# Performance work log

Measured on AMD Instinct MI355X. Metric: run time of the kernel, lower is better.

The kernel has to match this reference:

```python
import jax, jax.numpy as jnp
import numpy as np


def setup_inputs() -> dict:
    key = jax.random.key(0)
    ks = jax.random.split(key, 8)
    B, C, H, W = 4, 512, 64, 64
    M = C // 8
    sq = 1.0 / np.sqrt(C)
    return {
        "x": jax.random.normal(ks[0], (B, C, H, W), jnp.float32),
        "Wq": jax.random.normal(ks[1], (M, C), jnp.float32) * sq,
        "bq": jnp.zeros((M,), jnp.float32),
        "Wk": jax.random.normal(ks[2], (M, C), jnp.float32) * sq,
        "bk": jnp.zeros((M,), jnp.float32),
        "Wv": jax.random.normal(ks[3], (C, C), jnp.float32) * sq,
        "bv": jnp.zeros((C,), jnp.float32),
        "gamma": jax.random.uniform(ks[4], (1,), jnp.float32),
    }


def reference(x, Wq, bq, Wk, bk, Wv, bv, gamma):
    B, C, H, W = x.shape
    N = H * W
    xf = x.reshape(B, C, N)  # flatten spatial -> [B, C, N]
    # 1x1 convs are channel-mixing matmuls
    q = jnp.einsum('mc,bcn->bmn', Wq, xf) + bq[None, :, None]  # [B, M, N]
    k = jnp.einsum('mc,bcn->bmn', Wk, xf) + bk[None, :, None]  # [B, M, N]
    v = jnp.einsum('dc,bcn->bdn', Wv, xf) + bv[None, :, None]  # [B, C, N]
    # sim[b,i,j] = <q[:, i], k[:, j]>, softmax over j
    sim = jnp.einsum('bmi,bmj->bij', q, k)  # [B, N, N]
    attn = jax.nn.softmax(sim, axis=-1)
    # feat[b,c,i] = sum_j v[b,c,j] * attn[b,i,j]
    feat = jnp.einsum('bcj,bij->bci', v, attn)  # [B, C, N]
    out = gamma[0] * feat.reshape(B, C, H, W) + x
    return out
```

## Files before the change

### kernel.cpp

```cpp
#include <hip/hip_runtime.h>

typedef _Float16 f16;
typedef _Float16 f16x8 __attribute__((ext_vector_type(8)));
typedef float    f32x4 __attribute__((ext_vector_type(4)));
typedef unsigned int u32x2 __attribute__((ext_vector_type(2)));

#define B_ 4
#define C_ 512
#define N_ 4096
#define M_ 64

__device__ __forceinline__ unsigned pk2(float a, float b) {
    union { f16 h[2]; unsigned u; } t;
    t.h[0] = (f16)a; t.h[1] = (f16)b;
    return t.u;
}

__global__ __launch_bounds__(256) void wcvt(
    const float* __restrict__ Wq, const float* __restrict__ Wk,
    const float* __restrict__ Wv, f16* __restrict__ Wf)
{
    const int e = (blockIdx.x * 256 + threadIdx.x) * 8;
    const float* src;
    int off;
    if (e < 32768)      { src = Wq; off = e; }
    else if (e < 65536) { src = Wk; off = e - 32768; }
    else                { src = Wv; off = e - 65536; }
    float4 a = *(const float4*)(src + off);
    float4 b = *(const float4*)(src + off + 4);
    f16x8 o;
    o[0]=(f16)a.x; o[1]=(f16)a.y; o[2]=(f16)a.z; o[3]=(f16)a.w;
    o[4]=(f16)b.x; o[5]=(f16)b.y; o[6]=(f16)b.z; o[7]=(f16)b.w;
    *(f16x8*)(Wf + e) = o;
}

__global__ __launch_bounds__(512) void qkv2(
    const f16* __restrict__ Wf, const float* __restrict__ x,
    const float* __restrict__ bq, const float* __restrict__ bk,
    const float* __restrict__ bv,
    f16* __restrict__ qt, f16* __restrict__ ktf, f16* __restrict__ vf)
{
    __shared__ float sX[2][64][65];
    __shared__ float sBias[640];

    const int tid  = threadIdx.x;
    const int w    = tid >> 6;
    const int lane = tid & 63;
    const int l15  = lane & 15;
    const int quad = lane >> 4;
    const int n0   = blockIdx.x * 64;
    const int b    = blockIdx.y;
    const int row0 = w * 80;

    for (int e = tid; e < 640; e += 512)
        sBias[e] = (e < 64) ? bq[e] : (e < 128) ? bk[e - 64] : bv[e - 128];

    {
        float4 g[2];
        #pragma unroll
        for (int i = 0; i < 2; ++i) {
            int e = i * 512 + tid, c = e >> 4, n4 = (e & 15) * 4;
            g[i] = *(const float4*)(x + ((size_t)(b * C_ + c)) * N_ + n0 + n4);
        }
        #pragma unroll
        for (int i = 0; i < 2; ++i) {
            int e = i * 512 + tid, c = e >> 4, n4 = (e & 15) * 4;
            sX[0][c][n4 + 0] = g[i].x; sX[0][c][n4 + 1] = g[i].y;
            sX[0][c][n4 + 2] = g[i].z; sX[0][c][n4 + 3] = g[i].w;
        }
    }

    f32x4 acc[5][4] = {};

    for (int t = 0; t < 8; ++t) {
        const int cur = t & 1, nxt = cur ^ 1;

        float4 gn[2];
        if (t < 7) {
            #pragma unroll
            for (int i = 0; i < 2; ++i) {
                int e = i * 512 + tid, c = e >> 4, n4 = (e & 15) * 4;
                gn[i] = *(const float4*)(x + ((size_t)(b * C_ + (t + 1) * 64 + c)) * N_ + n0 + n4);
            }
        }

        __syncthreads();

        f16x8 af[5][2];
        #pragma unroll
        for (int ot = 0; ot < 5; ++ot)
            #pragma unroll
            for (int kh = 0; kh < 2; ++kh)
                af[ot][kh] = *(const f16x8*)(Wf + (size_t)(row0 + ot * 16 + l15) * 512
                                             + t * 64 + kh * 32 + quad * 8);

        f16x8 bf[4][2];
        #pragma unroll
        for (int nt = 0; nt < 4; ++nt)
            #pragma unroll
            for (int kh = 0; kh < 2; ++kh) {
                f16x8 o;
                #pragma unroll
                for (int jj = 0; jj < 8; ++jj)
                    o[jj] = (f16)sX[cur][kh * 32 + quad * 8 + jj][nt * 16 + l15];
                bf[nt][kh] = o;
            }

        #pragma unroll
        for (int ot = 0; ot < 5; ++ot)
            #pragma unroll
            for (int kh = 0; kh < 2; ++kh)
                #pragma unroll
                for (int nt = 0; nt < 4; ++nt)
                    acc[ot][nt] = __builtin_amdgcn_mfma_f32_16x16x32_f16(
                        af[ot][kh], bf[nt][kh], acc[ot][nt], 0, 0, 0);

        if (t < 7) {
            #pragma unroll
            for (int i = 0; i < 2; ++i) {
                int e = i * 512 + tid, c = e >> 4, n4 = (e & 15) * 4;
                sX[nxt][c][n4 + 0] = gn[i].x; sX[nxt][c][n4 + 1] = gn[i].y;
                sX[nxt][c][n4 + 2] = gn[i].z; sX[nxt][c][n4 + 3] = gn[i].w;
            }
        }
    }

    #pragma unroll
    for (int ot = 0; ot < 5; ++ot) {
        const int rowBase = row0 + ot * 16;
        const int rq = rowBase + quad * 4;
        #pragma unroll
        for (int nt = 0; nt < 4; ++nt) {
            const int n = n0 + nt * 16 + l15;
            union { f16 h[4]; unsigned long long u; } pkv;
            #pragma unroll
            for (int r = 0; r < 4; ++r)
                pkv.h[r] = (f16)(acc[ot][nt][r] + sBias[rq + r]);
            if (rowBase < 64) {
                *(unsigned long long*)(qt + ((size_t)(b * N_ + n)) * M_ + rq) = pkv.u;
            } else if (rowBase < 128) {
                const int ol = rq - 64;
                size_t idx = (((size_t)b * 256 + (n >> 4)) * 2 + (ol >> 5)) * 512
                           + (size_t)((((ol >> 3) & 3) * 16 + (n & 15)) * 8) + (ol & 7);
                *(unsigned long long*)(ktf + idx) = pkv.u;
            } else {
                const int c = rq - 128;
                #pragma unroll
                for (int r = 0; r < 4; ++r) {
                    size_t idx = ((size_t)b * (C_ * N_)) + (size_t)((c + r) >> 4) * 65536
                               + (size_t)(n >> 6) * 1024 + (size_t)((n >> 5) & 1) * 512
                               + (size_t)((((n >> 3) & 3) * 16 + ((c + r) & 15)) * 8) + (n & 7);
                    vf[idx] = pkv.h[r];
                }
            }
        }
    }
}

__global__ __launch_bounds__(512, 2) void attn(
    const f16* __restrict__ qt, const f16* __restrict__ ktf,
    const f16* __restrict__ vf, const float* __restrict__ x,
    const float* __restrict__ gamma, float* __restrict__ out)
{
    __shared__ __align__(16) char Pb[2][8192];
    __shared__ float mxs[8][4][16];
    __shared__ float lss[8][4][16];

    const int tid  = threadIdx.x;
    const int w    = tid >> 6;
    const int lane = tid & 63;
    const int l15  = lane & 15;
    const int quad = lane >> 4;
    const int jt   = w & 3;
    const int ish  = w >> 2;
    const int is0  = ish * 2, is1 = is0 + 1;

    const int lin  = blockIdx.x;
    const int b    = (lin & 7) >> 1;
    const int iblk = ((lin >> 3) << 1) | (lin & 1);
    const int i0   = iblk * 64;

    const f16* kln = ktf + (size_t)b * (N_ * M_) + lane * 8;
    const f16* vln = vf  + (size_t)b * (C_ * N_) + lane * 8;

    f16x8 bqf[4][2];
    #pragma unroll
    for (int is = 0; is < 4; ++is)
        #pragma unroll
        for (int kh = 0; kh < 2; ++kh)
            bqf[is][kh] = *(const f16x8*)(qt + ((size_t)(b * N_ + i0 + is * 16 + l15)) * M_
                                          + kh * 32 + quad * 8);

    float mx[4];
    #pragma unroll
    for (int is = 0; is < 4; ++is) mx[is] = -3.0e38f;
    {
        const f16* kw = kln + (size_t)(w * 512) * 64;
        f16x8 akc[4][2];
        #pragma unroll
        for (int t = 0; t < 4; ++t)
            #pragma unroll
            for (int kh = 0; kh < 2; ++kh)
                akc[t][kh] = *(const f16x8*)(kw + t * 1024 + kh * 512);

        #pragma unroll 2
        for (int jj = 0; jj < 512; jj += 64) {
            f16x8 akn[4][2];
            if (jj + 64 < 512) {
                const f16* kn = kw + (size_t)(jj + 64) * 64;
                #pragma unroll
                for (int t = 0; t < 4; ++t)
                    #pragma unroll
                    for (int kh = 0; kh < 2; ++kh)
                        akn[t][kh] = *(const f16x8*)(kn + t * 1024 + kh * 512);
            }
            #pragma unroll
            for (int t = 0; t < 4; ++t) {
                #pragma unroll
                for (int is = 0; is < 4; ++is) {
                    f32x4 s = {};
                    s = __builtin_amdgcn_mfma_f32_16x16x32_f16(akc[t][0], bqf[is][0], s, 0, 0, 0);
                    s = __builtin_amdgcn_mfma_f32_16x16x32_f16(akc[t][1], bqf[is][1], s, 0, 0, 0);
                    mx[is] = fmaxf(mx[is], fmaxf(fmaxf(s[0], s[1]), fmaxf(s[2], s[3])));
                }
            }
            #pragma unroll
            for (int t = 0; t < 4; ++t)
                #pragma unroll
                for (int kh = 0; kh < 2; ++kh)
                    akc[t][kh] = akn[t][kh];
        }
    }
    #pragma unroll
    for (int is = 0; is < 4; ++is) {
        mx[is] = fmaxf(mx[is], __shfl_xor(mx[is], 16, 64));
        mx[is] = fmaxf(mx[is], __shfl_xor(mx[is], 32, 64));
    }
    if (lane < 16) {
        #pragma unroll
        for (int is = 0; is < 4; ++is) mxs[w][is][lane] = mx[is];
    }
    __syncthreads();
    float m0 = -3.0e38f, m1 = -3.0e38f;
    #pragma unroll
    for (int w2 = 0; w2 < 8; ++w2) {
        m0 = fmaxf(m0, mxs[w2][is0][l15]);
        m1 = fmaxf(m1, mxs[w2][is1][l15]);
    }

    f32x4 acc[4][4] = {};
    float lp0 = 0.f, lp1 = 0.f;

    char* pbB = (char*)&Pb[0][0];
    const int swz = (l15 & 7) << 4;
    const int wb0 = ((is0 * 16 + l15) * 128 + (jt * 16 + quad * 4) * 2) ^ swz;
    const int wb1 = wb0 + 2048;
    int rb[4][2];
    #pragma unroll
    for (int is = 0; is < 4; ++is)
        #pragma unroll
        for (int kh = 0; kh < 2; ++kh)
            rb[is][kh] = ((is * 16 + l15) * 128 + kh * 64 + quad * 16) ^ swz;

    const f16* kp = kln + (size_t)(jt * 16) * 64;
    const int cw = w * 4;

    f16x8 ak0 = *(const f16x8*)(kp);
    f16x8 ak1 = *(const f16x8*)(kp + 512);
    {
        f32x4 s0 = {}, s1 = {};
        s0 = __builtin_amdgcn_mfma_f32_16x16x32_f16(ak0, bqf[is0][0], s0, 0, 0, 0);
        s0 = __builtin_amdgcn_mfma_f32_16x16x32_f16(ak1, bqf[is0][1], s0, 0, 0, 0);
        s1 = __builtin_amdgcn_mfma_f32_16x16x32_f16(ak0, bqf[is1][0], s1, 0, 0, 0);
        s1 = __builtin_amdgcn_mfma_f32_16x16x32_f16(ak1, bqf[is1][1], s1, 0, 0, 0);
        float p0 = __expf(s0[0] - m0), p1 = __expf(s0[1] - m0);
        float p2 = __expf(s0[2] - m0), p3 = __expf(s0[3] - m0);
        lp0 += (p0 + p1) + (p2 + p3);
        u32x2 pw0 = { pk2(p0, p1), pk2(p2, p3) };
        *(u32x2*)(pbB + wb0) = pw0;
        float q0 = __expf(s1[0] - m1), q1 = __expf(s1[1] - m1);
        float q2 = __expf(s1[2] - m1), q3 = __expf(s1[3] - m1);
        lp1 += (q0 + q1) + (q2 + q3);
        u32x2 pw1 = { pk2(q0, q1), pk2(q2, q3) };
        *(u32x2*)(pbB + wb1) = pw1;
    }
    ak0 = *(const f16x8*)(kp + 4096);
    ak1 = *(const f16x8*)(kp + 4096 + 512);
    f16x8 vc0[4], vc1[4];
    #pragma unroll
    for (int ct = 0; ct < 4; ++ct) {
        vc0[ct] = *(const f16x8*)(vln + (size_t)(cw + ct) * 65536);
        vc1[ct] = *(const f16x8*)(vln + (size_t)(cw + ct) * 65536 + 512);
    }
    __syncthreads();

    #pragma unroll 2
    for (int t = 0; t < 63; ++t) {
        const int cb = (t & 1) * 8192;
        const int nb = ((t + 1) & 1) * 8192;

        f16x8 pbf[4][2];
        #pragma unroll
        for (int is = 0; is < 4; ++is)
            #pragma unroll
            for (int kh = 0; kh < 2; ++kh)
                pbf[is][kh] = *(const f16x8*)(pbB + cb + rb[is][kh]);

        f32x4 s0 = {}, s1 = {};
        s0 = __builtin_amdgcn_mfma_f32_16x16x32_f16(ak0, bqf[is0][0], s0, 0, 0, 0);
        s0 = __builtin_amdgcn_mfma_f32_16x16x32_f16(ak1, bqf[is0][1], s0, 0, 0, 0);
        s1 = __builtin_amdgcn_mfma_f32_16x16x32_f16(ak0, bqf[is1][0], s1, 0, 0, 0);
        s1 = __builtin_amdgcn_mfma_f32_16x16x32_f16(ak1, bqf[is1][1], s1, 0, 0, 0);

        if (t + 2 < 64) {
            ak0 = *(const f16x8*)(kp + (size_t)(t + 2) * 4096);
            ak1 = *(const f16x8*)(kp + (size_t)(t + 2) * 4096 + 512);
        }
        const f16* vt = vln + (size_t)(t + 1) * 1024;
        f16x8 vn0[4], vn1[4];
        #pragma unroll
        for (int ct = 0; ct < 4; ++ct) {
            vn0[ct] = *(const f16x8*)(vt + (size_t)(cw + ct) * 65536);
            vn1[ct] = *(const f16x8*)(vt + (size_t)(cw + ct) * 65536 + 512);
        }

        {
            float p0 = __expf(s0[0] - m0), p1 = __expf(s0[1] - m0);
            float p2 = __expf(s0[2] - m0), p3 = __expf(s0[3] - m0);
            lp0 += (p0 + p1) + (p2 + p3);
            u32x2 pw = { pk2(p0, p1), pk2(p2, p3) };
            *(u32x2*)(pbB + nb + wb0) = pw;
        }
        {
            float q0 = __expf(s1[0] - m1), q1 = __expf(s1[1] - m1);
            float q2 = __expf(s1[2] - m1), q3 = __expf(s1[3] - m1);
            lp1 += (q0 + q1) + (q2 + q3);
            u32x2 pw = { pk2(q0, q1), pk2(q2, q3) };
            *(u32x2*)(pbB + nb + wb1) = pw;
        }

        __builtin_amdgcn_s_setprio(1);
        #pragma unroll
        for (int ct = 0; ct < 4; ++ct)
            #pragma unroll
            for (int is = 0; is < 4; ++is)
                acc[ct][is] = __builtin_amdgcn_mfma_f32_16x16x32_f16(vc0[ct], pbf[is][0], acc[ct][is], 0, 0, 0);
        #pragma unroll
        for (int ct = 0; ct < 4; ++ct)
            #pragma unroll
            for (int is = 0; is < 4; ++is)
                acc[ct][is] = __builtin_amdgcn_mfma_f32_16x16x32_f16(vc1[ct], pbf[is][1], acc[ct][is], 0, 0, 0);
        __builtin_amdgcn_s_setprio(0);

        __syncthreads();

        #pragma unroll
        for (int ct = 0; ct < 4; ++ct) { vc0[ct] = vn0[ct]; vc1[ct] = vn1[ct]; }
    }

    {
        const int cb = (63 & 1) * 8192;
        f16x8 pbf[4][2];
        #pragma unroll
        for (int is = 0; is < 4; ++is)
            #pragma unroll
            for (int kh = 0; kh < 2; ++kh)
                pbf[is][kh] = *(const f16x8*)(pbB + cb + rb[is][kh]);
        #pragma unroll
        for (int ct = 0; ct < 4; ++ct)
            #pragma unroll
            for (int is = 0; is < 4; ++is)
                acc[ct][is] = __builtin_amdgcn_mfma_f32_16x16x32_f16(vc0[ct], pbf[is][0], acc[ct][is], 0, 0, 0);
        #pragma unroll
        for (int ct = 0; ct < 4; ++ct)
            #pragma unroll
            for (int is = 0; is < 4; ++is)
                acc[ct][is] = __builtin_amdgcn_mfma_f32_16x16x32_f16(vc1[ct], pbf[is][1], acc[ct][is], 0, 0, 0);
    }

    lp0 += __shfl_xor(lp0, 16, 64);
    lp0 += __shfl_xor(lp0, 32, 64);
    lp1 += __shfl_xor(lp1, 16, 64);
    lp1 += __shfl_xor(lp1, 32, 64);
    if (lane < 16) { lss[w][is0][lane] = lp0; lss[w][is1][lane] = lp1; }
    __syncthreads();

    float linv[4];
    #pragma unroll
    for (int is = 0; is < 4; ++is) {
        const int wb = (is >> 1) * 4;
        float l = (lss[wb + 0][is][l15] + lss[wb + 1][is][l15])
                + (lss[wb + 2][is][l15] + lss[wb + 3][is][l15]);
        linv[is] = 1.0f / l;
    }

    const float g = gamma[0];
    #pragma unroll
    for (int is = 0; is < 4; ++is) {
        const int i = i0 + is * 16 + l15;
        #pragma unroll
        for (int ct = 0; ct < 4; ++ct) {
            #pragma unroll
            for (int r = 0; r < 4; ++r) {
                const int c = w * 64 + ct * 16 + quad * 4 + r;
                const size_t idx = ((size_t)(b * C_ + c)) * N_ + i;
                out[idx] = g * (acc[ct][is][r] * linv[is]) + x[idx];
            }
        }
    }
}

extern "C" void kernel_launch(void* const* d_in, const int* in_sizes, int n_in,
                              void* d_out, int out_size, void* d_ws, size_t ws_size,
                              hipStream_t stream)
{
    const float* x     = (const float*)d_in[0];
    const float* Wq    = (const float*)d_in[1];
    const float* bq    = (const float*)d_in[2];
    const float* Wk    = (const float*)d_in[3];
    const float* bk    = (const float*)d_in[4];
    const float* Wv    = (const float*)d_in[5];
    const float* bv    = (const float*)d_in[6];
    const float* gamma = (const float*)d_in[7];
    float* out = (float*)d_out;

    char* ws = (char*)d_ws;
    f16* qt  = (f16*)ws;
    f16* ktf = qt + (size_t)B_ * N_ * M_;
    f16* vf  = ktf + (size_t)B_ * N_ * M_;
    f16* Wf  = vf + (size_t)B_ * C_ * N_;

    wcvt<<<dim3(160), 256, 0, stream>>>(Wq, Wk, Wv, Wf);
    qkv2<<<dim3(N_ / 64, B_), 512, 0, stream>>>(Wf, x, bq, bk, bv, qt, ktf, vf);
    attn<<<dim3(256), 512, 0, stream>>>(qt, ktf, vf, x, gamma, out);
}
```

Measured before the change: 224.2 us.

## Store x tile as swizzled fp16 in LDS and prefetch weight fragments

The qkv projection kernel now converts x to fp16 before staging it in shared memory. Each thread loads 8 channels for one spatial column, which it writes as a single 16-byte vector into an XOR-swizzled layout, so B fragments come back as one vector LDS read instead of eight scalar float reads with conversions. Weight A fragments for the next k-step are also prefetched into registers and double-buffered alongside the x tile. This adds register pressure, and the global loads of x become scalar per-lane reads instead of float4.

```diff
diff --git a/kernel.cpp b/kernel.cpp
--- a/kernel.cpp
+++ b/kernel.cpp
@@ -40,7 +40,7 @@
     const float* __restrict__ bv,
     f16* __restrict__ qt, f16* __restrict__ ktf, f16* __restrict__ vf)
 {
-    __shared__ float sX[2][64][65];
+    __shared__ __align__(16) char sH[2][8192];
     __shared__ float sBias[640];
 
     const int tid  = threadIdx.x;
@@ -55,56 +55,64 @@
     for (int e = tid; e < 640; e += 512)
         sBias[e] = (e < 64) ? bq[e] : (e < 128) ? bk[e - 64] : bv[e - 128];
 
+    const int wbyte = (lane * 128 + w * 16) ^ ((lane & 7) << 4);
+    int rbyte[4][2];
+    #pragma unroll
+    for (int nt = 0; nt < 4; ++nt) {
+        const int n = nt * 16 + l15;
+        #pragma unroll
+        for (int kh = 0; kh < 2; ++kh)
+            rbyte[nt][kh] = (n * 128 + kh * 64 + quad * 16) ^ ((n & 7) << 4);
+    }
+
+    const float* xg = x + (size_t)b * (C_ * N_) + n0 + lane;
+    const f16*   wp = Wf + (size_t)row0 * 512 + quad * 8;
+
     {
-        float4 g[2];
-        #pragma unroll
-        for (int i = 0; i < 2; ++i) {
-            int e = i * 512 + tid, c = e >> 4, n4 = (e & 15) * 4;
-            g[i] = *(const float4*)(x + ((size_t)(b * C_ + c)) * N_ + n0 + n4);
-        }
-        #pragma unroll
-        for (int i = 0; i < 2; ++i) {
-            int e = i * 512 + tid, c = e >> 4, n4 = (e & 15) * 4;
-            sX[0][c][n4 + 0] = g[i].x; sX[0][c][n4 + 1] = g[i].y;
-            sX[0][c][n4 + 2] = g[i].z; sX[0][c][n4 + 3] = g[i].w;
-        }
-    }
+        float g[8];
+        #pragma unroll
+        for (int u = 0; u < 8; ++u)
+            g[u] = xg[(size_t)(w * 8 + u) * N_];
+        f16x8 h;
+        #pragma unroll
+        for (int u = 0; u < 8; ++u) h[u] = (f16)g[u];
+        *(f16x8*)(&sH[0][0] + wbyte) = h;
+    }
+    f16x8 afc[5][2];
+    #pragma unroll
+    for (int ot = 0; ot < 5; ++ot)
+        #pragma unroll
+        for (int kh = 0; kh < 2; ++kh)
+            afc[ot][kh] = *(const f16x8*)(wp + (size_t)(ot * 16 + l15) * 512 + kh * 32);
 
     f32x4 acc[5][4] = {};
 
     for (int t = 0; t < 8; ++t) {
-        const int cur = t & 1, nxt = cur ^ 1;
-
-        float4 gn[2];
+        char* sc = &sH[t & 1][0];
+        char* sn = &sH[(t & 1) ^ 1][0];
+
+        float gn[8];
+        f16x8 afn[5][2];
         if (t < 7) {
             #pragma unroll
-            for (int i = 0; i < 2; ++i) {
-                int e = i * 512 + tid, c = e >> 4, n4 = (e & 15) * 4;
-                gn[i] = *(const float4*)(x + ((size_t)(b * C_ + (t + 1) * 64 + c)) * N_ + n0 + n4);
-            }
+            for (int u = 0; u < 8; ++u)
+                gn[u] = xg[(size_t)((t + 1) * 64 + w * 8 + u) * N_];
+            #pragma unroll
+            for (int ot = 0; ot < 5; ++ot)
+                #pragma unroll
+                for (int kh = 0; kh < 2; ++kh)
+                    afn[ot][kh] = *(const f16x8*)(wp + (size_t)(ot * 16 + l15) * 512
+                                                  + (t + 1) * 64 + kh * 32);
         }
 
         __syncthreads();
 
-        f16x8 af[5][2];
-        #pragma unroll
-        for (int ot = 0; ot < 5; ++ot)
+        f16x8 bf[4][2];
+        #pragma unroll
+        for (int nt = 0; nt < 4; ++nt)
             #pragma unroll
             for (int kh = 0; kh < 2; ++kh)
-                af[ot][kh] = *(const f16x8*)(Wf + (size_t)(row0 + ot * 16 + l15) * 512
-                                             + t * 64 + kh * 32 + quad * 8);
-
-        f16x8 bf[4][2];
-        #pragma unroll
-        for (int nt = 0; nt < 4; ++nt)
-            #pragma unroll
-            for (int kh = 0; kh < 2; ++kh) {
-                f16x8 o;
-                #pragma unroll
-                for (int jj = 0; jj < 8; ++jj)
-                    o[jj] = (f16)sX[cur][kh * 32 + quad * 8 + jj][nt * 16 + l15];
-                bf[nt][kh] = o;
-            }
+                bf[nt][kh] = *(const f16x8*)(sc + rbyte[nt][kh]);
 
         #pragma unroll
         for (int ot = 0; ot < 5; ++ot)
@@ -113,15 +121,18 @@
                 #pragma unroll
                 for (int nt = 0; nt < 4; ++nt)
                     acc[ot][nt] = __builtin_amdgcn_mfma_f32_16x16x32_f16(
-                        af[ot][kh], bf[nt][kh], acc[ot][nt], 0, 0, 0);
+                        afc[ot][kh], bf[nt][kh], acc[ot][nt], 0, 0, 0);
 
         if (t < 7) {
-            #pragma unroll
-            for (int i = 0; i < 2; ++i) {
-                int e = i * 512 + tid, c = e >> 4, n4 = (e & 15) * 4;
-                sX[nxt][c][n4 + 0] = gn[i].x; sX[nxt][c][n4 + 1] = gn[i].y;
-                sX[nxt][c][n4 + 2] = gn[i].z; sX[nxt][c][n4 + 3] = gn[i].w;
-            }
+            f16x8 h;
+            #pragma unroll
+            for (int u = 0; u < 8; ++u) h[u] = (f16)gn[u];
+            *(f16x8*)(sn + wbyte) = h;
+            #pragma unroll
+            for (int ot = 0; ot < 5; ++ot)
+                #pragma unroll
+                for (int kh = 0; kh < 2; ++kh)
+                    afc[ot][kh] = afn[ot][kh];
         }
     }
 
```

After: 215.2 us. -4.0%, faster.

## Halve QKV projection tile and stage x as swizzled fp16 in shared memory

Applied to the files above, without the earlier changes.

The QKV projection kernel now processes 32 spatial positions per block instead of 64, which doubles the grid to 512 blocks and raises occupancy via launch bounds. The x tile is converted to fp16 once when stored and kept in an XOR-swizzled byte layout, so B fragments become single vector LDS reads instead of eight scalar float reads plus conversions. Weight fragments are loaded per output tile inside the loop to cut register pressure. In exchange, every weight fragment is reloaded twice as often across blocks, and global x loads become scalar strided reads.

```diff
diff --git a/kernel.cpp b/kernel.cpp
--- a/kernel.cpp
+++ b/kernel.cpp
@@ -1,6 +1,7 @@
 #include <hip/hip_runtime.h>
 
 typedef _Float16 f16;
+typedef _Float16 f16x4 __attribute__((ext_vector_type(4)));
 typedef _Float16 f16x8 __attribute__((ext_vector_type(8)));
 typedef float    f32x4 __attribute__((ext_vector_type(4)));
 typedef unsigned int u32x2 __attribute__((ext_vector_type(2)));
@@ -34,13 +35,13 @@
     *(f16x8*)(Wf + e) = o;
 }
 
-__global__ __launch_bounds__(512) void qkv2(
+__global__ __launch_bounds__(512, 4) void qkv3(
     const f16* __restrict__ Wf, const float* __restrict__ x,
     const float* __restrict__ bq, const float* __restrict__ bk,
     const float* __restrict__ bv,
     f16* __restrict__ qt, f16* __restrict__ ktf, f16* __restrict__ vf)
 {
-    __shared__ float sX[2][64][65];
+    __shared__ __align__(16) char sH[2][4096];
     __shared__ float sBias[640];
 
     const int tid  = threadIdx.x;
@@ -48,80 +49,78 @@
     const int lane = tid & 63;
     const int l15  = lane & 15;
     const int quad = lane >> 4;
-    const int n0   = blockIdx.x * 64;
+    const int n0   = blockIdx.x * 32;
     const int b    = blockIdx.y;
     const int row0 = w * 80;
 
     for (int e = tid; e < 640; e += 512)
         sBias[e] = (e < 64) ? bq[e] : (e < 128) ? bk[e - 64] : bv[e - 128];
 
+    const int sn  = tid & 31;
+    const int scg = tid >> 5;
+    const int wbyte = (sn * 128 + scg * 8) ^ ((sn & 7) << 4);
+    int rbyte[2][2];
+    #pragma unroll
+    for (int nt = 0; nt < 2; ++nt)
+        #pragma unroll
+        for (int kh = 0; kh < 2; ++kh)
+            rbyte[nt][kh] = ((nt * 16 + l15) * 128 + kh * 64 + quad * 16)
+                            ^ ((l15 & 7) << 4);
+
+    const float* xg = x + (size_t)b * (C_ * N_) + n0 + sn;
+    const f16*   wp = Wf + (size_t)row0 * 512 + quad * 8;
+
     {
-        float4 g[2];
-        #pragma unroll
-        for (int i = 0; i < 2; ++i) {
-            int e = i * 512 + tid, c = e >> 4, n4 = (e & 15) * 4;
-            g[i] = *(const float4*)(x + ((size_t)(b * C_ + c)) * N_ + n0 + n4);
-        }
-        #pragma unroll
-        for (int i = 0; i < 2; ++i) {
-            int e = i * 512 + tid, c = e >> 4, n4 = (e & 15) * 4;
-            sX[0][c][n4 + 0] = g[i].x; sX[0][c][n4 + 1] = g[i].y;
-            sX[0][c][n4 + 2] = g[i].z; sX[0][c][n4 + 3] = g[i].w;
-        }
-    }
-
-    f32x4 acc[5][4] = {};
+        float g[4];
+        #pragma unroll
+        for (int i = 0; i < 4; ++i)
+            g[i] = xg[(size_t)(scg * 4 + i) * N_];
+        f16x4 h;
+        #pragma unroll
+        for (int i = 0; i < 4; ++i) h[i] = (f16)g[i];
+        *(f16x4*)(&sH[0][0] + wbyte) = h;
+    }
+
+    f32x4 acc[5][2] = {};
 
     for (int t = 0; t < 8; ++t) {
-        const int cur = t & 1, nxt = cur ^ 1;
-
-        float4 gn[2];
+        char* sc = &sH[t & 1][0];
+        char* so = &sH[(t & 1) ^ 1][0];
+
+        float gn[4];
         if (t < 7) {
             #pragma unroll
-            for (int i = 0; i < 2; ++i) {
-                int e = i * 512 + tid, c = e >> 4, n4 = (e & 15) * 4;
-                gn[i] = *(const float4*)(x + ((size_t)(b * C_ + (t + 1) * 64 + c)) * N_ + n0 + n4);
+            for (int i = 0; i < 4; ++i)
+                gn[i] = xg[(size_t)((t + 1) * 64 + scg * 4 + i) * N_];
+        }
+
+        __syncthreads();
+
+        f16x8 bf[2][2];
+        #pragma unroll
+        for (int nt = 0; nt < 2; ++nt)
+            #pragma unroll
+            for (int kh = 0; kh < 2; ++kh)
+                bf[nt][kh] = *(const f16x8*)(sc + rbyte[nt][kh]);
+
+        #pragma unroll
+        for (int ot = 0; ot < 5; ++ot) {
+            f16x8 af0 = *(const f16x8*)(wp + (size_t)(ot * 16 + l15) * 512 + t * 64);
+            f16x8 af1 = *(const f16x8*)(wp + (size_t)(ot * 16 + l15) * 512 + t * 64 + 32);
+            #pragma unroll
+            for (int nt = 0; nt < 2; ++nt) {
+                acc[ot][nt] = __builtin_amdgcn_mfma_f32_16x16x32_f16(
+                    af0, bf[nt][0], acc[ot][nt], 0, 0, 0);
+                acc[ot][nt] = __builtin_amdgcn_mfma_f32_16x16x32_f16(
+                    af1, bf[nt][1], acc[ot][nt], 0, 0, 0);
             }
         }
 
-        __syncthreads();
-
-        f16x8 af[5][2];
-        #pragma unroll
-        for (int ot = 0; ot < 5; ++ot)
-            #pragma unroll
-            for (int kh = 0; kh < 2; ++kh)
-                af[ot][kh] = *(const f16x8*)(Wf + (size_t)(row0 + ot * 16 + l15) * 512
-                                             + t * 64 + kh * 32 + quad * 8);
-
-        f16x8 bf[4][2];
-        #pragma unroll
-        for (int nt = 0; nt < 4; ++nt)
-            #pragma unroll
-            for (int kh = 0; kh < 2; ++kh) {
-                f16x8 o;
-                #pragma unroll
-                for (int jj = 0; jj < 8; ++jj)
-                    o[jj] = (f16)sX[cur][kh * 32 + quad * 8 + jj][nt * 16 + l15];
-                bf[nt][kh] = o;
-            }
-
-        #pragma unroll
-        for (int ot = 0; ot < 5; ++ot)
-            #pragma unroll
-            for (int kh = 0; kh < 2; ++kh)
-                #pragma unroll
-                for (int nt = 0; nt < 4; ++nt)
-                    acc[ot][nt] = __builtin_amdgcn_mfma_f32_16x16x32_f16(
-                        af[ot][kh], bf[nt][kh], acc[ot][nt], 0, 0, 0);
-
         if (t < 7) {
-            #pragma unroll
-            for (int i = 0; i < 2; ++i) {
-                int e = i * 512 + tid, c = e >> 4, n4 = (e & 15) * 4;
-                sX[nxt][c][n4 + 0] = gn[i].x; sX[nxt][c][n4 + 1] = gn[i].y;
-                sX[nxt][c][n4 + 2] = gn[i].z; sX[nxt][c][n4 + 3] = gn[i].w;
-            }
+            f16x4 h;
+            #pragma unroll
+            for (int i = 0; i < 4; ++i) h[i] = (f16)gn[i];
+            *(f16x4*)(so + wbyte) = h;
         }
     }
 
@@ -130,7 +129,7 @@
         const int rowBase = row0 + ot * 16;
         const int rq = rowBase + quad * 4;
         #pragma unroll
-        for (int nt = 0; nt < 4; ++nt) {
+        for (int nt = 0; nt < 2; ++nt) {
             const int n = n0 + nt * 16 + l15;
             union { f16 h[4]; unsigned long long u; } pkv;
             #pragma unroll
@@ -431,6 +430,6 @@
     f16* Wf  = vf + (size_t)B_ * C_ * N_;
 
     wcvt<<<dim3(160), 256, 0, stream>>>(Wq, Wk, Wv, Wf);
-    qkv2<<<dim3(N_ / 64, B_), 512, 0, stream>>>(Wf, x, bq, bk, bv, qt, ktf, vf);
+    qkv3<<<dim3(N_ / 32, B_), 512, 0, stream>>>(Wf, x, bq, bk, bv, qt, ktf, vf);
     attn<<<dim3(256), 512, 0, stream>>>(qt, ktf, vf, x, gamma, out);
 }
```

New measurement: 234.9 us. 4.8% more time.
